# Kernel optimization log

Measured on AMD Instinct MI355X. Metric: run time of the kernel, lower is better.

Reference implementation:

```python
import jax, jax.numpy as jnp
import numpy as np

B, S, D = 8, 1024, 1024
H, DH = 16, 64  # num_attention_heads, attention_head_size; H*DH == D


def setup_inputs() -> dict:
    key = jax.random.key(0)
    ks = jax.random.split(key, 6)
    scale = 0.02
    return {
        "hidden_states": jax.random.normal(ks[0], (B, S, D), jnp.float32),
        "right_hidden_states": jax.random.normal(ks[1], (B, S, D), jnp.float32),
        "attention_mask": jnp.ones((B, S, S), jnp.float32),
        "Wq": jax.random.normal(ks[2], (D, H * DH), jnp.float32) * scale,
        "bq": jnp.zeros((H * DH,), jnp.float32),
        "Wk": jax.random.normal(ks[3], (D, H * DH), jnp.float32) * scale,
        "bk": jnp.zeros((H * DH,), jnp.float32),
        "Wv": jax.random.normal(ks[4], (D, H * DH), jnp.float32) * scale,
        "bv": jnp.zeros((H * DH,), jnp.float32),
    }


def _split_heads(x, b):
    # (B, S, H*DH) -> (B, H, S, DH)
    return x.reshape(b, -1, H, DH).transpose(0, 2, 1, 3)


def reference(hidden_states, right_hidden_states, attention_mask, Wq, bq, Wk, bk, Wv, bv):
    b = hidden_states.shape[0]
    q = _split_heads(hidden_states @ Wq + bq, b)          # (B,H,Sq,DH)
    k = _split_heads(right_hidden_states @ Wk + bk, b)    # (B,H,Sk,DH)
    v = _split_heads(right_hidden_states @ Wv + bv, b)    # (B,H,Sk,DH)

    scores = jnp.einsum("bhqd,bhkd->bhqk", q, k) / jnp.sqrt(jnp.asarray(DH, q.dtype))
    scores = jnp.sum(scores, axis=1, keepdims=True)       # (B,1,Sq,Sk) head-summed

    ext = (1.0 - attention_mask[:, None, :, :].astype(scores.dtype)) * -1e9
    probs = jax.nn.softmax(scores + ext, axis=-1)         # (B,1,Sq,Sk)

    ctx = jnp.matmul(probs, v)                            # broadcast -> (B,H,Sq,DH)
    # Faithful to original: reshape WITHOUT transposing heads back.
    return ctx.reshape(b, -1, H * DH)                     # (B,Sq,H*DH)
```

## Files before the change

### kernel.cpp

```cpp
#include <hip/hip_runtime.h>
#include <stdint.h>

constexpr int S = 1024;
constexpr int D = 1024;
constexpr int NB = 8;

typedef __bf16 bf16x8 __attribute__((ext_vector_type(8)));
typedef float floatx4 __attribute__((ext_vector_type(4)));

#define AS1 __attribute__((address_space(1)))
#define AS3 __attribute__((address_space(3)))

__device__ __forceinline__ unsigned short f2bf(float f) {
  unsigned u = __builtin_bit_cast(unsigned, f);
  u += 0x7fffu + ((u >> 16) & 1u);
  return (unsigned short)(u >> 16);
}

__device__ __forceinline__ float bf2f(unsigned short x) {
  unsigned u = ((unsigned)x) << 16;
  return __builtin_bit_cast(float, u);
}

__device__ __forceinline__ void gload16(const void* g, void* l) {
  __builtin_amdgcn_global_load_lds((const AS1 unsigned int*)g, (AS3 unsigned int*)l, 16, 0, 0);
}

__global__ __launch_bounds__(256) void prep_kernel(
    const float4* __restrict__ hs4, const float4* __restrict__ rhs4,
    ushort4* __restrict__ hsb4, ushort4* __restrict__ rhsb4, int n4,
    const float* __restrict__ Wq, const float* __restrict__ Wk, const float* __restrict__ Wv,
    unsigned short* __restrict__ WvT, ushort4* __restrict__ Wqb4, ushort4* __restrict__ Wkb4,
    const float* __restrict__ bq, const float* __restrict__ bk, float* __restrict__ u,
    float* __restrict__ v, float* __restrict__ cbuf) {
  __shared__ float tile[32][33];
  const int bid = blockIdx.x;
  if (bid < 16384) {
    int i = bid * 256 + threadIdx.x;
    const float4* src;
    ushort4* dst;
    int j;
    if (i < n4) {
      src = hs4; dst = hsb4; j = i;
    } else {
      src = rhs4; dst = rhsb4; j = i - n4;
    }
    float4 w = src[j];
    ushort4 o;
    o.x = f2bf(w.x); o.y = f2bf(w.y); o.z = f2bf(w.z); o.w = f2bf(w.w);
    dst[j] = o;
  } else if (bid < 18432) {
    int j = (bid - 16384) * 256 + threadIdx.x;
    const float4* src = (j < 262144) ? (const float4*)Wq : (const float4*)Wk;
    ushort4* dst = (j < 262144) ? Wqb4 : Wkb4;
    int jj = (j < 262144) ? j : j - 262144;
    float4 w = src[jj];
    ushort4 o;
    o.x = f2bf(w.x); o.y = f2bf(w.y); o.z = f2bf(w.z); o.w = f2bf(w.w);
    dst[jj] = o;
  } else if (bid < 19456) {
    const int r = bid - 18432;
    const int bx = (r & 31) * 32;
    const int by = (r >> 5) * 32;
    const int x = threadIdx.x & 31;
    const int y0 = threadIdx.x >> 5;
    for (int i = 0; i < 4; ++i) {
      int y = y0 + i * 8;
      tile[y][x] = Wv[(by + y) * D + bx + x];
    }
    __syncthreads();
    for (int i = 0; i < 4; ++i) {
      int y = y0 + i * 8;
      WvT[(long long)(bx + y) * D + by + x] = f2bf(tile[x][y]);
    }
  } else if (bid < 19460) {
    const int d = (bid - 19456) * 256 + threadIdx.x;
    const float* row = Wq + (long long)d * 1024;
    float s = 0.f;
    for (int c = 0; c < 1024; ++c) s += row[c] * bk[c];
    u[d] = 0.125f * s;
  } else if (bid < 19464) {
    const int d = (bid - 19460) * 256 + threadIdx.x;
    const float* row = Wk + (long long)d * 1024;
    float s = 0.f;
    for (int c = 0; c < 1024; ++c) s += row[c] * bq[c];
    v[d] = 0.125f * s;
  } else {
    __shared__ float sh[256];
    const int tid = threadIdx.x;
    float s = 0.f;
    for (int c = tid; c < 1024; c += 256) s += bq[c] * bk[c];
    sh[tid] = s;
    __syncthreads();
    for (int o = 128; o; o >>= 1) {
      if (tid < o) sh[tid] += sh[tid + o];
      __syncthreads();
    }
    if (tid == 0) cbuf[0] = 0.125f * sh[0];
  }
}


#define GEMM_STAGE_SETUP(Abase, lda_, Bbase, ldb_)                            \
  const int srow = tid >> 2;                                                  \
  const int scg = (((tid & 3) ^ ((srow >> 1) & 3)) * 8);                      \
  const unsigned short* aG0 = (Abase) + (long long)srow * (lda_) + scg;       \
  const unsigned short* aG1 = aG0 + (long long)64 * (lda_);                   \
  const unsigned short* bG0 = (Bbase) + (long long)srow * (ldb_) + scg;       \
  const unsigned short* bG1 = bG0 + (long long)64 * (ldb_);                   \
  unsigned short* aL0 = As + w * 512;                                         \
  unsigned short* aL1 = As + w * 512 + 2048;                                  \
  unsigned short* bL0 = Bs + w * 512;                                         \
  unsigned short* bL1 = Bs + w * 512 + 2048;

#define GEMM_KLOOP(Klen)                                                               \
  for (int k0 = 0; k0 < (Klen); k0 += 32) {                                            \
    gload16(aG0 + k0, aL0);                                                            \
    gload16(aG1 + k0, aL1);                                                            \
    gload16(bG0 + k0, bL0);                                                            \
    gload16(bG1 + k0, bL1);                                                            \
    __syncthreads();                                                                   \
    bf16x8 af[4], bfr[4];                                                              \
    for (int t = 0; t < 4; ++t) {                                                      \
      af[t] = *reinterpret_cast<const bf16x8*>(As + (wm + t * 16 + r15) * 32 + pq);    \
      bfr[t] = *reinterpret_cast<const bf16x8*>(Bs + (wn + t * 16 + r15) * 32 + pq);   \
    }                                                                                  \
    for (int mt = 0; mt < 4; ++mt)                                                     \
      for (int nt = 0; nt < 4; ++nt)                                                   \
        acc[mt][nt] =                                                                  \
            __builtin_amdgcn_mfma_f32_16x16x32_bf16(af[mt], bfr[nt], acc[mt][nt], 0, 0, 0); \
    __syncthreads();                                                                   \
  }

#define GEMM_COMMON_IDX                  \
  const int tid = threadIdx.x;           \
  const int lane = tid & 63;             \
  const int w = tid >> 6;                \
  const int r15 = lane & 15;             \
  const int quad = lane >> 4;            \
  const int pq = (quad ^ ((r15 >> 1) & 3)) * 8; \
  const int wm = (w >> 1) * 64;          \
  const int wn = (w & 1) * 64;

#define GEMM_ACC_INIT                    \
  floatx4 acc[4][4];                     \
  for (int i = 0; i < 4; ++i)            \
    for (int j = 0; j < 4; ++j) acc[i][j] = {0.f, 0.f, 0.f, 0.f};

__global__ __launch_bounds__(256) void wprod_kernel(
    const unsigned short* __restrict__ Wkb, const unsigned short* __restrict__ Wqb,
    float* __restrict__ Mtf, const unsigned short* __restrict__ hsb,
    const unsigned short* __restrict__ rhsb, const float* __restrict__ u,
    const float* __restrict__ v, const float* __restrict__ cbuf, float* __restrict__ t2,
    float* __restrict__ t3) {
  __shared__ __align__(16) unsigned short As[128 * 32];
  __shared__ __align__(16) unsigned short Bs[128 * 32];
  const int bid = blockIdx.x;
  if (bid < 256) {
    GEMM_COMMON_IDX
    const int tilei = bid & 63;
    const int kc = bid >> 6;
    const int bx = tilei & 7;
    const int by = tilei >> 3;
    const unsigned short* A = Wkb + (long long)by * 128 * D + kc * 256;
    const unsigned short* Bt = Wqb + (long long)bx * 128 * D + kc * 256;
    GEMM_STAGE_SETUP(A, D, Bt, D)
    GEMM_ACC_INIT
    GEMM_KLOOP(256)
    float* dst = Mtf + ((long long)kc << 20);
    for (int mt = 0; mt < 4; ++mt)
      for (int nt = 0; nt < 4; ++nt) {
        const int mrow = by * 128 + wm + mt * 16 + quad * 4;
        const int nc = bx * 128 + wn + nt * 16 + r15;
        floatx4 vv = acc[mt][nt];
        for (int e = 0; e < 4; ++e) dst[(long long)(mrow + e) * 1024 + nc] = vv[e] * 0.125f;
      }
  } else {
    const int tid = threadIdx.x;
    const bool isT2 = bid < 288;
    const int row = (isT2 ? (bid - 256) : (bid - 288)) * 256 + tid;
    const float* vec = isT2 ? u : v;
    const unsigned short* mat = isT2 ? hsb : rhsb;
    float* out = isT2 ? t2 : t3;
    __shared__ int nz;
    if (tid == 0) nz = 0;
    __syncthreads();
    const float4* u4 = (const float4*)vec;
    float4 uu = u4[tid];
    if (uu.x != 0.f || uu.y != 0.f || uu.z != 0.f || uu.w != 0.f) nz = 1;
    __syncthreads();
    const float c2 = 0.5f * cbuf[0];
    if (!nz) {
      out[row] = c2;
      return;
    }
    const ushort4* r4 = (const ushort4*)(mat + (long long)row * 1024);
    float s = 0.f;
    for (int c4 = 0; c4 < 256; ++c4) {
      ushort4 h = r4[c4];
      s += bf2f(h.x) * vec[c4 * 4 + 0] + bf2f(h.y) * vec[c4 * 4 + 1] +
           bf2f(h.z) * vec[c4 * 4 + 2] + bf2f(h.w) * vec[c4 * 4 + 3];
    }
    out[row] = s + c2;
  }
}

__global__ __launch_bounds__(256) void castM_kernel(const float4* __restrict__ Mtf4,
                                                    ushort4* __restrict__ Mtb4) {
  const int j = blockIdx.x * 256 + threadIdx.x;
  float4 a = Mtf4[j];
  float4 b = Mtf4[j + 262144];
  float4 c = Mtf4[j + 524288];
  float4 d = Mtf4[j + 786432];
  ushort4 o;
  o.x = f2bf(a.x + b.x + c.x + d.x);
  o.y = f2bf(a.y + b.y + c.y + d.y);
  o.z = f2bf(a.z + b.z + c.z + d.z);
  o.w = f2bf(a.w + b.w + c.w + d.w);
  Mtb4[j] = o;
}

__global__ __launch_bounds__(256) void gemm_fused_kernel(
    const unsigned short* __restrict__ hsb, const unsigned short* __restrict__ rhsb,
    const unsigned short* __restrict__ Mtb, const unsigned short* __restrict__ WvT,
    const float* __restrict__ bv, unsigned short* __restrict__ hsMb,
    unsigned short* __restrict__ Vmt) {
  __shared__ __align__(16) unsigned short As[128 * 32];
  __shared__ __align__(16) unsigned short Bs[128 * 32];
  GEMM_COMMON_IDX
  const int seg = (int)(blockIdx.x >> 3);
  const long long nloc = (blockIdx.x & 7) * 128;
  const long long m0 = (long long)blockIdx.y * 128;
  const unsigned short* A = ((seg == 0) ? hsb : rhsb) + m0 * D;
  const unsigned short* Bt = ((seg == 0) ? Mtb : WvT) + nloc * D;

  GEMM_STAGE_SETUP(A, D, Bt, D)
  GEMM_ACC_INIT
  GEMM_KLOOP(D)

  for (int mt = 0; mt < 4; ++mt) {
    for (int nt = 0; nt < 4; ++nt) {
      const long long mrow = m0 + wm + mt * 16 + quad * 4;
      const long long nc = nloc + wn + nt * 16 + r15;
      floatx4 vv = acc[mt][nt];
      if (seg == 0) {
        for (int e = 0; e < 4; ++e) hsMb[(mrow + e) * D + nc] = f2bf(vv[e]);
      } else {
        const float bval = bv[nc];
        for (int e = 0; e < 4; ++e) {
          long long m = mrow + e;
          Vmt[(m >> 10) * (long long)(S * D) + nc * S + (m & 1023)] = f2bf(vv[e] + bval);
        }
      }
    }
  }
}

__global__ __launch_bounds__(256) void gemm_scores_kernel(
    const unsigned short* __restrict__ hsMb, const unsigned short* __restrict__ rhsb,
    const float* __restrict__ mask, unsigned short* __restrict__ E, float* __restrict__ rowsumP,
    const float* __restrict__ t2, const float* __restrict__ t3) {
  __shared__ __align__(16) unsigned short As[128 * 32];
  __shared__ __align__(16) unsigned short Bs[128 * 32];
  GEMM_COMMON_IDX
  const int bid = blockIdx.x;
  const int z = bid & 7;
  const int r = bid >> 3;
  const int by = r >> 3;
  const int bx = r & 7;
  const long long m0 = (long long)by * 128;
  const long long n0 = (long long)bx * 128;
  const unsigned short* A = hsMb + (long long)z * S * D + m0 * D;
  const unsigned short* Bt = rhsb + (long long)z * S * D + n0 * D;

  GEMM_STAGE_SETUP(A, D, Bt, D)
  GEMM_ACC_INIT
  GEMM_KLOOP(D)

  const long long zE = (long long)z * S * 1024;
  float rowpart[4][4];
  for (int mt = 0; mt < 4; ++mt)
    for (int e = 0; e < 4; ++e) rowpart[mt][e] = 0.f;

  for (int mt = 0; mt < 4; ++mt) {
    for (int nt = 0; nt < 4; ++nt) {
      const long long mrow = m0 + wm + mt * 16 + quad * 4;
      const long long nc = n0 + wn + nt * 16 + r15;
      const float t3v = t3[z * 1024 + nc];
      floatx4 vv = acc[mt][nt];
      for (int e = 0; e < 4; ++e) {
        long long m = mrow + e;
        float mval = mask[zE + m * 1024 + nc];
        float sc = vv[e] + t2[z * 1024 + m] + t3v + (1.0f - mval) * -1e9f;
        float Ev = __expf(sc);
        E[zE + m * 1024 + nc] = f2bf(Ev);
        rowpart[mt][e] += Ev;
      }
    }
  }
  const int slot = (bx << 11) + ((wn >> 6) << 10);
  for (int mt = 0; mt < 4; ++mt) {
    for (int e = 0; e < 4; ++e) {
      float s = rowpart[mt][e];
      s += __shfl_xor(s, 1, 64);
      s += __shfl_xor(s, 2, 64);
      s += __shfl_xor(s, 4, 64);
      s += __shfl_xor(s, 8, 64);
      if (r15 == 0) {
        int mloc = (int)(m0 + wm + mt * 16 + quad * 4 + e);
        rowsumP[(z << 14) + slot + mloc] = s;
      }
    }
  }
}

__global__ __launch_bounds__(256) void gemm_ctx_kernel(const unsigned short* __restrict__ E,
                                                       const unsigned short* __restrict__ Vmt,
                                                       const float* __restrict__ rowsumP,
                                                       float* __restrict__ out) {
  __shared__ __align__(16) unsigned short As[128 * 32];
  __shared__ __align__(16) unsigned short Bs[128 * 32];
  __shared__ float rsinv[128];
  GEMM_COMMON_IDX
  const int bid = blockIdx.x;
  const int z = bid & 7;
  const int r = bid >> 3;
  const int by = r >> 3;
  const int bx = r & 7;
  const long long m0 = (long long)by * 128;
  const long long n0 = (long long)bx * 128;
  const unsigned short* A = E + (long long)z * S * 1024 + m0 * 1024;
  const unsigned short* Bt = Vmt + (long long)z * S * D + n0 * D;

  if (tid < 128) {
    float s = 0.f;
    for (int t = 0; t < 16; ++t) s += rowsumP[(z << 14) + (t << 10) + (int)m0 + tid];
    rsinv[tid] = 1.0f / s;
  }

  GEMM_STAGE_SETUP(A, 1024, Bt, D)
  GEMM_ACC_INIT
  GEMM_KLOOP(1024)

  for (int mt = 0; mt < 4; ++mt) {
    for (int nt = 0; nt < 4; ++nt) {
      const int r0 = wm + mt * 16 + quad * 4;
      const long long ncol = n0 + wn + nt * 16 + r15;
      floatx4 vv = acc[mt][nt];
      for (int e = 0; e < 4; ++e) {
        long long m = m0 + r0 + e;
        float val = vv[e] * rsinv[r0 + e];
        out[(long long)z * S * D + (ncol >> 6) * (long long)(S * 64) + m * 64 + (ncol & 63)] =
            val;
      }
    }
  }
}

extern "C" void kernel_launch(void* const* d_in, const int* in_sizes, int n_in, void* d_out,
                              int out_size, void* d_ws, size_t ws_size, hipStream_t stream) {
  const float* hs = (const float*)d_in[0];
  const float* rhs = (const float*)d_in[1];
  const float* mask = (const float*)d_in[2];
  const float* Wq = (const float*)d_in[3];
  const float* bq = (const float*)d_in[4];
  const float* Wk = (const float*)d_in[5];
  const float* bk = (const float*)d_in[6];
  const float* Wv = (const float*)d_in[7];
  const float* bv = (const float*)d_in[8];
  float* out = (float*)d_out;
  char* ws = (char*)d_ws;
  const size_t MB = 1ull << 20;
  unsigned short* WvT = (unsigned short*)(ws + 0 * MB);
  unsigned short* Wqb = (unsigned short*)(ws + 2 * MB);
  unsigned short* Wkb = (unsigned short*)(ws + 4 * MB);
  unsigned short* Mtb = (unsigned short*)(ws + 6 * MB);
  float* u = (float*)(ws + 8 * MB);
  float* v = (float*)(ws + 8 * MB + 4096);
  float* cbuf = (float*)(ws + 8 * MB + 8192);
  float* t2 = (float*)(ws + 8 * MB + 16384);
  float* t3 = (float*)(ws + 8 * MB + 49152);
  float* rowsumP = (float*)(ws + 8 * MB + 131072);
  unsigned short* hsb = (unsigned short*)(ws + 9 * MB);
  unsigned short* rhsb = (unsigned short*)(ws + 25 * MB);
  unsigned short* hsMb = (unsigned short*)(ws + 41 * MB);
  float* Mtf = (float*)(ws + 41 * MB);
  unsigned short* Vmt = (unsigned short*)(ws + 57 * MB);
  unsigned short* E = (unsigned short*)(ws + 9 * MB);

  const int n4 = NB * S * D / 4;
  prep_kernel<<<19465, 256, 0, stream>>>((const float4*)hs, (const float4*)rhs, (ushort4*)hsb,
                                         (ushort4*)rhsb, n4, Wq, Wk, Wv, WvT, (ushort4*)Wqb,
                                         (ushort4*)Wkb, bq, bk, u, v, cbuf);

  wprod_kernel<<<320, 256, 0, stream>>>(Wkb, Wqb, Mtf, hsb, rhsb, u, v, cbuf, t2, t3);
  castM_kernel<<<1024, 256, 0, stream>>>((const float4*)Mtf, (ushort4*)Mtb);

  gemm_fused_kernel<<<dim3(16, 64), 256, 0, stream>>>(hsb, rhsb, Mtb, WvT, bv, hsMb, Vmt);

  gemm_scores_kernel<<<512, 256, 0, stream>>>(hsMb, rhsb, mask, E, rowsumP, t2, t3);

  gemm_ctx_kernel<<<512, 256, 0, stream>>>(E, Vmt, rowsumP, out);
}
```

Measured before the change: 309.7 us.

## Use 64-wide K steps in main GEMMs, drop split-K wprod and cast kernel

The three large GEMM kernels now stage two 32-wide K slices per iteration into doubled LDS buffers, which halves the number of barrier pairs per K loop. The Wk·Wq product no longer uses split-K with an fp32 partial buffer and a separate cast/reduce kernel. Instead 64 blocks each compute a full-K tile and write bf16 directly, which removes one launch and the fp32 round trip. The fused projection GEMM also gets a block-index swizzle for better L2 locality. The costs are doubled LDS use per block, which may lower occupancy, and only 64 GEMM blocks doing the weight product serially over K.

```diff
diff --git a/kernel.cpp b/kernel.cpp
--- a/kernel.cpp
+++ b/kernel.cpp
@@ -101,7 +101,22 @@
 }
 
 
-#define GEMM_STAGE_SETUP(Abase, lda_, Bbase, ldb_)                            \
+#define GEMM_COMMON_IDX                  \
+  const int tid = threadIdx.x;           \
+  const int lane = tid & 63;             \
+  const int w = tid >> 6;                \
+  const int r15 = lane & 15;             \
+  const int quad = lane >> 4;            \
+  const int pq = (quad ^ ((r15 >> 1) & 3)) * 8; \
+  const int wm = (w >> 1) * 64;          \
+  const int wn = (w & 1) * 64;
+
+#define GEMM_ACC_INIT                    \
+  floatx4 acc[4][4];                     \
+  for (int i = 0; i < 4; ++i)            \
+    for (int j = 0; j < 4; ++j) acc[i][j] = {0.f, 0.f, 0.f, 0.f};
+
+#define GEMM_STAGE_SETUP32(Abase, lda_, Bbase, ldb_)                          \
   const int srow = tid >> 2;                                                  \
   const int scg = (((tid & 3) ^ ((srow >> 1) & 3)) * 8);                      \
   const unsigned short* aG0 = (Abase) + (long long)srow * (lda_) + scg;       \
@@ -113,7 +128,7 @@
   unsigned short* bL0 = Bs + w * 512;                                         \
   unsigned short* bL1 = Bs + w * 512 + 2048;
 
-#define GEMM_KLOOP(Klen)                                                               \
+#define GEMM_KLOOP32(Klen)                                                             \
   for (int k0 = 0; k0 < (Klen); k0 += 32) {                                            \
     gload16(aG0 + k0, aL0);                                                            \
     gload16(aG1 + k0, aL1);                                                            \
@@ -132,53 +147,69 @@
     __syncthreads();                                                                   \
   }
 
-#define GEMM_COMMON_IDX                  \
-  const int tid = threadIdx.x;           \
-  const int lane = tid & 63;             \
-  const int w = tid >> 6;                \
-  const int r15 = lane & 15;             \
-  const int quad = lane >> 4;            \
-  const int pq = (quad ^ ((r15 >> 1) & 3)) * 8; \
-  const int wm = (w >> 1) * 64;          \
-  const int wn = (w & 1) * 64;
-
-#define GEMM_ACC_INIT                    \
-  floatx4 acc[4][4];                     \
-  for (int i = 0; i < 4; ++i)            \
-    for (int j = 0; j < 4; ++j) acc[i][j] = {0.f, 0.f, 0.f, 0.f};
+#define GEMM_STAGE_SETUP64(Abase, lda_, Bbase, ldb_)                          \
+  const int srow = tid >> 2;                                                  \
+  const int scg = (((tid & 3) ^ ((srow >> 1) & 3)) * 8);                      \
+  const unsigned short* aG0 = (Abase) + (long long)srow * (lda_) + scg;       \
+  const unsigned short* aG1 = aG0 + (long long)64 * (lda_);                   \
+  const unsigned short* bG0 = (Bbase) + (long long)srow * (ldb_) + scg;       \
+  const unsigned short* bG1 = bG0 + (long long)64 * (ldb_);
+
+#define GEMM_KLOOP64(Klen)                                                               \
+  for (int k0 = 0; k0 < (Klen); k0 += 64) {                                              \
+    gload16(aG0 + k0, As[0] + w * 512);                                                  \
+    gload16(aG1 + k0, As[0] + w * 512 + 2048);                                           \
+    gload16(aG0 + k0 + 32, As[1] + w * 512);                                             \
+    gload16(aG1 + k0 + 32, As[1] + w * 512 + 2048);                                      \
+    gload16(bG0 + k0, Bs[0] + w * 512);                                                  \
+    gload16(bG1 + k0, Bs[0] + w * 512 + 2048);                                           \
+    gload16(bG0 + k0 + 32, Bs[1] + w * 512);                                             \
+    gload16(bG1 + k0 + 32, Bs[1] + w * 512 + 2048);                                      \
+    __syncthreads();                                                                     \
+    for (int h = 0; h < 2; ++h) {                                                        \
+      bf16x8 af[4], bfr[4];                                                              \
+      for (int t = 0; t < 4; ++t) {                                                      \
+        af[t] = *reinterpret_cast<const bf16x8*>(As[h] + (wm + t * 16 + r15) * 32 + pq); \
+        bfr[t] = *reinterpret_cast<const bf16x8*>(Bs[h] + (wn + t * 16 + r15) * 32 + pq);\
+      }                                                                                  \
+      for (int mt = 0; mt < 4; ++mt)                                                     \
+        for (int nt = 0; nt < 4; ++nt)                                                   \
+          acc[mt][nt] =                                                                  \
+              __builtin_amdgcn_mfma_f32_16x16x32_bf16(af[mt], bfr[nt], acc[mt][nt], 0, 0, 0); \
+    }                                                                                    \
+    __syncthreads();                                                                     \
+  }
 
 __global__ __launch_bounds__(256) void wprod_kernel(
     const unsigned short* __restrict__ Wkb, const unsigned short* __restrict__ Wqb,
-    float* __restrict__ Mtf, const unsigned short* __restrict__ hsb,
+    unsigned short* __restrict__ Mtb, const unsigned short* __restrict__ hsb,
     const unsigned short* __restrict__ rhsb, const float* __restrict__ u,
     const float* __restrict__ v, const float* __restrict__ cbuf, float* __restrict__ t2,
     float* __restrict__ t3) {
   __shared__ __align__(16) unsigned short As[128 * 32];
   __shared__ __align__(16) unsigned short Bs[128 * 32];
   const int bid = blockIdx.x;
-  if (bid < 256) {
+  if (bid < 64) {
     GEMM_COMMON_IDX
-    const int tilei = bid & 63;
-    const int kc = bid >> 6;
-    const int bx = tilei & 7;
-    const int by = tilei >> 3;
-    const unsigned short* A = Wkb + (long long)by * 128 * D + kc * 256;
-    const unsigned short* Bt = Wqb + (long long)bx * 128 * D + kc * 256;
-    GEMM_STAGE_SETUP(A, D, Bt, D)
+    const int bx = bid & 7;
+    const int by = bid >> 3;
+    const unsigned short* A = Wkb + (long long)by * 128 * D;
+    const unsigned short* Bt = Wqb + (long long)bx * 128 * D;
+    GEMM_STAGE_SETUP32(A, D, Bt, D)
     GEMM_ACC_INIT
-    GEMM_KLOOP(256)
-    float* dst = Mtf + ((long long)kc << 20);
+    GEMM_KLOOP32(D)
     for (int mt = 0; mt < 4; ++mt)
       for (int nt = 0; nt < 4; ++nt) {
         const int mrow = by * 128 + wm + mt * 16 + quad * 4;
         const int nc = bx * 128 + wn + nt * 16 + r15;
         floatx4 vv = acc[mt][nt];
-        for (int e = 0; e < 4; ++e) dst[(long long)(mrow + e) * 1024 + nc] = vv[e] * 0.125f;
+        for (int e = 0; e < 4; ++e)
+          Mtb[(long long)(mrow + e) * 1024 + nc] = f2bf(vv[e] * 0.125f);
       }
   } else {
     const int tid = threadIdx.x;
-    const bool isT2 = bid < 288;
-    const int row = (isT2 ? (bid - 256) : (bid - 288)) * 256 + tid;
+    const bool isT2 = bid < 96;
+    const int row = (isT2 ? (bid - 64) : (bid - 96)) * 256 + tid;
     const float* vec = isT2 ? u : v;
     const unsigned short* mat = isT2 ? hsb : rhsb;
     float* out = isT2 ? t2 : t3;
@@ -205,38 +236,27 @@
   }
 }
 
-__global__ __launch_bounds__(256) void castM_kernel(const float4* __restrict__ Mtf4,
-                                                    ushort4* __restrict__ Mtb4) {
-  const int j = blockIdx.x * 256 + threadIdx.x;
-  float4 a = Mtf4[j];
-  float4 b = Mtf4[j + 262144];
-  float4 c = Mtf4[j + 524288];
-  float4 d = Mtf4[j + 786432];
-  ushort4 o;
-  o.x = f2bf(a.x + b.x + c.x + d.x);
-  o.y = f2bf(a.y + b.y + c.y + d.y);
-  o.z = f2bf(a.z + b.z + c.z + d.z);
-  o.w = f2bf(a.w + b.w + c.w + d.w);
-  Mtb4[j] = o;
-}
-
 __global__ __launch_bounds__(256) void gemm_fused_kernel(
     const unsigned short* __restrict__ hsb, const unsigned short* __restrict__ rhsb,
     const unsigned short* __restrict__ Mtb, const unsigned short* __restrict__ WvT,
     const float* __restrict__ bv, unsigned short* __restrict__ hsMb,
     unsigned short* __restrict__ Vmt) {
-  __shared__ __align__(16) unsigned short As[128 * 32];
-  __shared__ __align__(16) unsigned short Bs[128 * 32];
+  __shared__ __align__(16) unsigned short As[2][4096];
+  __shared__ __align__(16) unsigned short Bs[2][4096];
   GEMM_COMMON_IDX
-  const int seg = (int)(blockIdx.x >> 3);
-  const long long nloc = (blockIdx.x & 7) * 128;
-  const long long m0 = (long long)blockIdx.y * 128;
+  const int bid = blockIdx.x;
+  const int swz = (bid & 7) * 128 + (bid >> 3);
+  const int bx = swz & 15;
+  const int by = swz >> 4;
+  const int seg = bx >> 3;
+  const long long nloc = (long long)(bx & 7) * 128;
+  const long long m0 = (long long)by * 128;
   const unsigned short* A = ((seg == 0) ? hsb : rhsb) + m0 * D;
   const unsigned short* Bt = ((seg == 0) ? Mtb : WvT) + nloc * D;
 
-  GEMM_STAGE_SETUP(A, D, Bt, D)
+  GEMM_STAGE_SETUP64(A, D, Bt, D)
   GEMM_ACC_INIT
-  GEMM_KLOOP(D)
+  GEMM_KLOOP64(D)
 
   for (int mt = 0; mt < 4; ++mt) {
     for (int nt = 0; nt < 4; ++nt) {
@@ -260,8 +280,8 @@
     const unsigned short* __restrict__ hsMb, const unsigned short* __restrict__ rhsb,
     const float* __restrict__ mask, unsigned short* __restrict__ E, float* __restrict__ rowsumP,
     const float* __restrict__ t2, const float* __restrict__ t3) {
-  __shared__ __align__(16) unsigned short As[128 * 32];
-  __shared__ __align__(16) unsigned short Bs[128 * 32];
+  __shared__ __align__(16) unsigned short As[2][4096];
+  __shared__ __align__(16) unsigned short Bs[2][4096];
   GEMM_COMMON_IDX
   const int bid = blockIdx.x;
   const int z = bid & 7;
@@ -273,9 +293,9 @@
   const unsigned short* A = hsMb + (long long)z * S * D + m0 * D;
   const unsigned short* Bt = rhsb + (long long)z * S * D + n0 * D;
 
-  GEMM_STAGE_SETUP(A, D, Bt, D)
+  GEMM_STAGE_SETUP64(A, D, Bt, D)
   GEMM_ACC_INIT
-  GEMM_KLOOP(D)
+  GEMM_KLOOP64(D)
 
   const long long zE = (long long)z * S * 1024;
   float rowpart[4][4];
@@ -318,8 +338,8 @@
                                                        const unsigned short* __restrict__ Vmt,
                                                        const float* __restrict__ rowsumP,
                                                        float* __restrict__ out) {
-  __shared__ __align__(16) unsigned short As[128 * 32];
-  __shared__ __align__(16) unsigned short Bs[128 * 32];
+  __shared__ __align__(16) unsigned short As[2][4096];
+  __shared__ __align__(16) unsigned short Bs[2][4096];
   __shared__ float rsinv[128];
   GEMM_COMMON_IDX
   const int bid = blockIdx.x;
@@ -338,9 +358,9 @@
     rsinv[tid] = 1.0f / s;
   }
 
-  GEMM_STAGE_SETUP(A, 1024, Bt, D)
+  GEMM_STAGE_SETUP64(A, 1024, Bt, D)
   GEMM_ACC_INIT
-  GEMM_KLOOP(1024)
+  GEMM_KLOOP64(1024)
 
   for (int mt = 0; mt < 4; ++mt) {
     for (int nt = 0; nt < 4; ++nt) {
@@ -384,7 +404,6 @@
   unsigned short* hsb = (unsigned short*)(ws + 9 * MB);
   unsigned short* rhsb = (unsigned short*)(ws + 25 * MB);
   unsigned short* hsMb = (unsigned short*)(ws + 41 * MB);
-  float* Mtf = (float*)(ws + 41 * MB);
   unsigned short* Vmt = (unsigned short*)(ws + 57 * MB);
   unsigned short* E = (unsigned short*)(ws + 9 * MB);
 
@@ -393,10 +412,9 @@
                                          (ushort4*)rhsb, n4, Wq, Wk, Wv, WvT, (ushort4*)Wqb,
                                          (ushort4*)Wkb, bq, bk, u, v, cbuf);
 
-  wprod_kernel<<<320, 256, 0, stream>>>(Wkb, Wqb, Mtf, hsb, rhsb, u, v, cbuf, t2, t3);
-  castM_kernel<<<1024, 256, 0, stream>>>((const float4*)Mtf, (ushort4*)Mtb);
-
-  gemm_fused_kernel<<<dim3(16, 64), 256, 0, stream>>>(hsb, rhsb, Mtb, WvT, bv, hsMb, Vmt);
+  wprod_kernel<<<128, 256, 0, stream>>>(Wkb, Wqb, Mtb, hsb, rhsb, u, v, cbuf, t2, t3);
+
+  gemm_fused_kernel<<<1024, 256, 0, stream>>>(hsb, rhsb, Mtb, WvT, bv, hsMb, Vmt);
 
   gemm_scores_kernel<<<512, 256, 0, stream>>>(hsMb, rhsb, mask, E, rowsumP, t2, t3);
 
```

Result: faster. 293.5 us (-5.2%).
